# Optimization experiments

Hardware: AMD Instinct MI355X
Metric: run time of the kernel (lower is better)

## Reference

```python
import jax, jax.numpy as jnp
import numpy as np

B, C, H, W = 4, 128, 128, 128
E, K, HID = 11, 6, 512  # num_experts, active_experts, 4*dim


def setup_inputs() -> dict:
    key = jax.random.key(0)
    ks = jax.random.split(key, 5)
    return {
        "x": jax.random.normal(ks[0], (B, C, H, W), jnp.float32),
        "gate_w": jax.random.normal(ks[1], (E, C), jnp.float32) * 0.02,
        "gate_b": jnp.zeros((E,), jnp.float32),
        "w1": jax.random.normal(ks[2], (E, HID, C), jnp.float32) * 0.02,
        "b1": jnp.zeros((E, HID), jnp.float32),
        "w2": jax.random.normal(ks[3], (E, C, HID), jnp.float32) * 0.02,
        "b2": jnp.zeros((E, C), jnp.float32),
    }


def reference(x, gate_w, gate_b, w1, b1, w2, b2):
    n_experts = gate_w.shape[0]
    k = K  # active_experts
    # channels-last for per-pixel routing / 1x1-conv-as-matmul
    xcl = jnp.transpose(x, (0, 2, 3, 1))  # [B,H,W,C]
    # --- router (1x1 conv gate + softmax over experts + top-k) ---
    logits = jnp.einsum('bhwc,ec->bhwe', xcl, gate_w) + gate_b
    scores = jax.nn.softmax(logits, axis=-1)            # [B,H,W,E]
    topk_p, topk_i = jax.lax.top_k(scores, k)           # [B,H,W,K]
    topk_p = topk_p / topk_p.sum(axis=-1, keepdims=True)
    # scatter routing weights into dense per-expert mask (indices distinct)
    onehot = jax.nn.one_hot(topk_i, n_experts, dtype=x.dtype)  # [B,H,W,K,E]
    mask = jnp.einsum('bhwke,bhwk->bhwe', onehot, topk_p)      # [B,H,W,E]
    # --- dense expert compute, masked accumulate (as in original loop) ---
    acc = jnp.zeros_like(xcl)
    for e in range(n_experts):
        h = jax.nn.gelu(jnp.einsum('bhwc,dc->bhwd', xcl, w1[e]) + b1[e],
                        approximate=False)  # torch GELU is exact erf form
        oe = jnp.einsum('bhwd,cd->bhwc', h, w2[e]) + b2[e]
        acc = acc + mask[..., e:e + 1] * oe
    y = x + jnp.transpose(acc, (0, 3, 1, 2))  # back to NCHW
    # --- load-balancing aux loss ---
    mean_prob = scores.mean(axis=(0, 1, 2))            # [E]
    mean_load = onehot.sum(axis=3).mean(axis=(0, 1, 2))  # binary mask mean, [E]
    aux_loss = n_experts * jnp.sum(mean_prob * mean_load)
    return (y, aux_loss)
```

## Files before the change

### kernel.cpp

```cpp
#include <hip/hip_runtime.h>
#include <stdint.h>

#define C_   128
#define HW_  16384
#define CHW_ (C_*HW_)
#define N_   65536
#define E_   11
#define K_   6
#define HID_ 512

typedef __attribute__((ext_vector_type(8))) _Float16 half8;
typedef __attribute__((ext_vector_type(2))) _Float16 h2;
typedef __attribute__((ext_vector_type(2))) __fp16 fp16v2;
typedef __attribute__((ext_vector_type(16))) float float16v;
typedef __attribute__((ext_vector_type(2))) unsigned uint2v;

#define GLD(g, s) __builtin_amdgcn_global_load_lds( \
    (const __attribute__((address_space(1))) unsigned int*)(uintptr_t)(g), \
    (__attribute__((address_space(3))) unsigned int*)(unsigned int)(uintptr_t)(s), 16, 0, 0)

__device__ __forceinline__ h2 pkrtz(float a, float b){
  union { fp16v2 f; h2 h; } u;
  u.f = __builtin_amdgcn_cvt_pkrtz(a, b);
  return u.h;
}
__device__ __forceinline__ h2 gelu2h(h2 v, h2 wr2){
  h2 u = v * v;
  h2 s = u * (h2)(_Float16)(-0.00076957f) + (h2)(_Float16)(0.0147811f);
  s = s * u + (h2)(_Float16)(-0.126434f);
  s = s * u + (h2)(_Float16)(0.795742f);
  h2 p = v * s;
  h2 phi = p * (h2)(_Float16)(0.5f) + (h2)(_Float16)(0.5f);
  return v * wr2 * phi;
}
__device__ __forceinline__ void pswap32(unsigned &a, unsigned &b){
#if __has_builtin(__builtin_amdgcn_permlane32_swap)
  uint2v r = __builtin_amdgcn_permlane32_swap(a, b, false, false);
  a = r.x; b = r.y;
#else
  asm volatile("v_permlane32_swap_b32 %0, %1" : "+v"(a), "+v"(b));
#endif
}

__global__ __launch_bounds__(256) void k_convert(const float* __restrict__ w1,
                                                 const float* __restrict__ w2,
                                                 const float* __restrict__ b1,
                                                 unsigned short* __restrict__ wimg,
                                                 unsigned short* __restrict__ b1h,
                                                 float* __restrict__ auxsum){
  int t = blockIdx.x * 256 + threadIdx.x;
  if (t < 23) auxsum[t] = 0.0f;
  if (t >= 185856) return;
  if (t >= 180224){
    int t2 = t - 180224;
    int rec = t2 >> 5, j5 = t2 & 31;
    int hi = j5 >> 4, j = j5 & 15;
    int e = rec >> 4, hc = rec & 15;
    int row = (j & 3) + 8 * (j >> 2) + 4 * hi;
    union { _Float16 h; unsigned short u; } cv;
    cv.h = (_Float16)b1[e * 512 + hc * 32 + row];
    b1h[rec * 32 + j5] = cv.u;
    return;
  }
  const float* src;
  size_t dst;
  if (t < 90112){
    int e = t >> 13, hid = (t >> 4) & 511, c8 = t & 15;
    src = w1 + (size_t)t * 8;
    int rec = e * 16 + (hid >> 5);
    int kc = c8 >> 1, half = c8 & 1;
    int l = (hid & 31) | (half << 5);
    dst = (size_t)rec * 8192 + kc * 512 + l * 8;
  } else {
    int u = t - 90112;
    int e = u >> 13, cc = (u >> 6) & 127, hd8 = u & 63;
    src = w2 + (size_t)u * 8;
    int rec = e * 16 + (hd8 >> 2);
    int kc2 = (hd8 >> 1) & 1, half = hd8 & 1, ct = cc >> 5;
    int l = (cc & 31) | (half << 5);
    dst = (size_t)rec * 8192 + 4096 + (ct * 2 + kc2) * 512 + l * 8;
  }
  float4 a = *(const float4*)src, b = *(const float4*)(src + 4);
  union { _Float16 h[8]; uint4 v; } u4;
  u4.h[0] = (_Float16)a.x; u4.h[1] = (_Float16)a.y;
  u4.h[2] = (_Float16)a.z; u4.h[3] = (_Float16)a.w;
  u4.h[4] = (_Float16)b.x; u4.h[5] = (_Float16)b.y;
  u4.h[6] = (_Float16)b.z; u4.h[7] = (_Float16)b.w;
  *(uint4*)(wimg + dst) = u4.v;
}

__global__ __launch_bounds__(256) void k_pre(const float* __restrict__ x,
                                             const float* __restrict__ gw,
                                             const float* __restrict__ gb,
                                             const float* __restrict__ b2,
                                             unsigned short* __restrict__ xcl,
                                             float* __restrict__ mask,
                                             float* __restrict__ auxsum){
  __shared__ __align__(16) float tt[64 * 130];
  __shared__ __align__(16) float g[E_ * C_];
  __shared__ float gbs[E_];
  __shared__ float ap[E_], al[E_];
  int tid = threadIdx.x;
  int pix0 = blockIdx.x * 64;
  int b = pix0 >> 14, hw0 = pix0 & 16383;
  const float* xb = x + (size_t)b * CHW_ + hw0;

  for (int i = tid; i < E_ * C_; i += 256) g[i] = gw[i];
  if (tid < E_) { gbs[tid] = gb[tid]; ap[tid] = 0.f; al[tid] = 0.f; }

  #pragma unroll 4
  for (int it = 0; it < 32; ++it){
    int flat = it * 256 + tid;
    int c = flat >> 6, p = flat & 63;
    tt[p * 130 + c] = xb[c * HW_ + p];
  }
  __syncthreads();
  #pragma unroll 4
  for (int it = 0; it < 16; ++it){
    int u = it * 256 + tid;
    int p = u >> 6, cc = u & 63;
    float f0 = tt[p * 130 + 2 * cc], f1 = tt[p * 130 + 2 * cc + 1];
    union { h2 h; unsigned u; } pv;
    pv.h = pkrtz(f0, f1);
    ((unsigned*)xcl)[(size_t)(pix0 + p) * 64 + cc] = pv.u;
  }

  int p = tid >> 2, t4 = tid & 3;
  float lg[E_];
  #pragma unroll
  for (int e = 0; e < E_; ++e) lg[e] = (t4 == 0) ? gbs[e] : 0.f;
  const float2* ttrow = (const float2*)(tt + p * 130 + t4 * 32);
  #pragma unroll 4
  for (int j2 = 0; j2 < 16; ++j2){
    float2 xv = ttrow[j2];
    #pragma unroll
    for (int e = 0; e < E_; ++e){
      float2 gv = *(const float2*)(g + e * C_ + t4 * 32 + j2 * 2);
      lg[e] = fmaf(xv.x, gv.x, lg[e]);
      lg[e] = fmaf(xv.y, gv.y, lg[e]);
    }
  }
  #pragma unroll
  for (int e = 0; e < E_; ++e){
    lg[e] += __shfl_xor(lg[e], 1, 64);
    lg[e] += __shfl_xor(lg[e], 2, 64);
  }
  float mx = lg[0];
  #pragma unroll
  for (int e = 1; e < E_; ++e) mx = fmaxf(mx, lg[e]);
  float pr[E_]; float s = 0.f;
  #pragma unroll
  for (int e = 0; e < E_; ++e){ pr[e] = expf(lg[e] - mx); s += pr[e]; }
  float inv = 1.0f / s;
  #pragma unroll
  for (int e = 0; e < E_; ++e) pr[e] *= inv;

  unsigned selmask = 0; float wsum = 0.f;
  for (int k = 0; k < K_; ++k){
    float bv = -1.f; int bi = 0;
    #pragma unroll
    for (int e = 0; e < E_; ++e){
      bool better = (((selmask >> e) & 1u) == 0u) && (pr[e] > bv);
      bv = better ? pr[e] : bv;
      bi = better ? e : bi;
    }
    selmask |= 1u << bi; wsum += bv;
  }
  float invw = 1.0f / wsum;
  if (t4 == 0){
    int pix = pix0 + p;
    #pragma unroll
    for (int e = 0; e < E_; ++e){
      bool sel = (selmask >> e) & 1u;
      mask[(size_t)pix * E_ + e] = sel ? pr[e] * invw : 0.f;
      atomicAdd(&ap[e], pr[e]);
      if (sel) atomicAdd(&al[e], 1.0f);
    }
  }
  __syncthreads();
  if (tid < E_){
    atomicAdd(&auxsum[tid], ap[tid]);
    atomicAdd(&auxsum[E_ + tid], al[tid]);
  }
  if (blockIdx.x == 0 && tid < 64){
    int nz = 0;
    for (int idx = tid; idx < E_ * C_; idx += 64)
      nz |= (__float_as_uint(b2[idx]) != 0u) ? 1 : 0;
    if (nz) atomicOr((int*)(auxsum + 22), 1);
  }
}

__global__ __launch_bounds__(512, 2) void k_ffn(const unsigned short* __restrict__ xcl,
                                                const unsigned short* __restrict__ wimg,
                                                const unsigned short* __restrict__ b1h,
                                                const float* __restrict__ b2,
                                                const float* __restrict__ mask,
                                                const float* __restrict__ aux,
                                                const float* __restrict__ x,
                                                float* __restrict__ y){
  __shared__ unsigned char smem[65536];
  int tid = threadIdx.x;
  int w = tid >> 6, l = tid & 63;
  int l31 = l & 31, hi = l >> 5;
  int hi4 = hi * 4;
  int pix0 = blockIdx.x * 256;
  int off = (blockIdx.x % 11) * 16;
  const unsigned char* wimgB = (const unsigned char*)wimg;
  const unsigned char* b1hB  = (const unsigned char*)b1h;

  if (blockIdx.x == 0 && tid == 0){
    float s = 0.f;
    const float invN = 1.0f / (float)N_;
    for (int e = 0; e < E_; ++e)
      s += (aux[e] * invN) * (aux[E_ + e] * invN);
    y[(size_t)N_ * C_] = (float)E_ * s;
  }

  half8 Xf[8];
  {
    const unsigned short* xrow = xcl + ((size_t)(pix0 + w * 32 + l31) << 7) + hi * 8;
    #pragma unroll
    for (int kc = 0; kc < 8; ++kc)
      Xf[kc] = *(const half8*)(xrow + kc * 16);
  }

  uint4 bhA[4], bhB[4];
  const size_t mrow = (size_t)(pix0 + w * 32 + l31) * 11;

  {
    #pragma unroll
    for (int k = 0; k < 2; ++k){
      int rec = off + k;
      const unsigned char* gs = wimgB + (size_t)rec * 16384 + w * 2048 + l * 16;
      unsigned char* dst = smem + k * 16384 + w * 2048;
      GLD(gs, dst);
      GLD(gs + 1024, dst + 1024);
      const unsigned char* bp = b1hB + rec * 64 + hi * 32;
      bhA[2 * k]     = *(const uint4*)(bp);
      bhA[2 * k + 1] = *(const uint4*)(bp + 16);
    }
  }
  float wrn = mask[mrow + (off >> 4)];
  __syncthreads();

  float16v facc[4];
  #pragma unroll
  for (int ct = 0; ct < 4; ++ct) facc[ct] = (float16v)0.0f;
  h2 wr2 = (h2)(_Float16)0.0f;

#define REC_BODY(WB, BH0, BH1)                                                      \
  {                                                                                 \
    float16v hacc_ = (float16v)0.0f;                                                \
    _Pragma("unroll")                                                               \
    for (int kc_ = 0; kc_ < 8; ++kc_){                                              \
      half8 a_ = *(const half8*)((WB) + kc_ * 1024 + l * 16);                       \
      hacc_ = __builtin_amdgcn_mfma_f32_32x32x16_f16(a_, Xf[kc_], hacc_, 0, 0, 0);  \
    }                                                                               \
    union { uint4 v[2]; h2 h[8]; } bu_;                                             \
    bu_.v[0] = BH0; bu_.v[1] = BH1;                                                 \
    unsigned pd_[8];                                                                \
    _Pragma("unroll")                                                               \
    for (int k_ = 0; k_ < 8; ++k_){                                                 \
      h2 v_ = pkrtz(hacc_[2 * k_], hacc_[2 * k_ + 1]);                              \
      v_ = v_ + bu_.h[k_];                                                          \
      union { h2 h; unsigned u; } g_;                                               \
      g_.h = gelu2h(v_, wr2);                                                       \
      pd_[k_] = g_.u;                                                               \
    }                                                                               \
    pswap32(pd_[0], pd_[2]); pswap32(pd_[1], pd_[3]);                               \
    pswap32(pd_[4], pd_[6]); pswap32(pd_[5], pd_[7]);                               \
    union { unsigned u[4]; half8 s; } cv0_, cv1_;                                   \
    cv0_.u[0] = pd_[0]; cv0_.u[1] = pd_[1]; cv0_.u[2] = pd_[2]; cv0_.u[3] = pd_[3]; \
    cv1_.u[0] = pd_[4]; cv1_.u[1] = pd_[5]; cv1_.u[2] = pd_[6]; cv1_.u[3] = pd_[7]; \
    _Pragma("unroll")                                                               \
    for (int ct_ = 0; ct_ < 4; ++ct_){                                              \
      half8 a0_ = *(const half8*)((WB) + 8192 + (ct_ * 2 + 0) * 1024 + l * 16);     \
      half8 a1_ = *(const half8*)((WB) + 8192 + (ct_ * 2 + 1) * 1024 + l * 16);     \
      facc[ct_] = __builtin_amdgcn_mfma_f32_32x32x16_f16(a0_, cv0_.s, facc[ct_], 0, 0, 0); \
      facc[ct_] = __builtin_amdgcn_mfma_f32_32x32x16_f16(a1_, cv1_.s, facc[ct_], 0, 0, 0); \
    }                                                                               \
  }

#define SUPER_BODY(J, BHC, BHL)                                                     \
  {                                                                                 \
    asm volatile("s_waitcnt vmcnt(4)" ::: "memory");                                \
    __builtin_amdgcn_s_barrier();                                                   \
    __builtin_amdgcn_sched_barrier(0);                                              \
         \
    {                                                                               \
      unsigned char* dbuf_ = smem + ((((J) + 1) & 1) << 15);                        \
      _Pragma("unroll")                                                             \
      for (int k_ = 0; k_ < 2; ++k_){                                               \
        int rn_ = 2 * (J) + 2 + k_ + off; if (rn_ >= 176) rn_ -= 176;               \
        const unsigned char* gs_ = wimgB + (size_t)rn_ * 16384 + w * 2048 + l * 16; \
        unsigned char* dst_ = dbuf_ + k_ * 16384 + w * 2048;                        \
        GLD(gs_, dst_);                                                             \
        GLD(gs_ + 1024, dst_ + 1024);                                               \
        const unsigned char* bp_ = b1hB + rn_ * 64 + hi * 32;                       \
        BHL[2 * k_]     = *(const uint4*)(bp_);                                     \
        BHL[2 * k_ + 1] = *(const uint4*)(bp_ + 16);                                \
      }                                                                             \
    }                                                                               \
    __builtin_amdgcn_sched_barrier(0);                                              \
    if (((J) & 7) == 0){           \
      _Float16 wh_ = (_Float16)wrn;                                                 \
      wr2 = (h2){wh_, wh_};                                                         \
      int rn_ = 2 * (J) + 16 + off; if (rn_ >= 176) rn_ -= 176;                     \
      wrn = mask[mrow + (rn_ >> 4)];                                                \
    }                                                                               \
    const unsigned char* wb_ = smem + (((J) & 1) << 15);                            \
    REC_BODY(wb_, BHC[0], BHC[1]);                                                  \
    REC_BODY(wb_ + 16384, BHC[2], BHC[3]);                                          \
  }

  #pragma unroll 1
  for (int jj = 0; jj < 44; ++jj){
    SUPER_BODY(2 * jj,     bhA, bhB);
    SUPER_BODY(2 * jj + 1, bhB, bhA);
  }
#undef SUPER_BODY
#undef REC_BODY

  __syncthreads();
  float* lds_t = (float*)smem;
  float* b2t   = (float*)(smem + 17408);
  for (int idx = tid; idx < 1536; idx += 512){
    int cc = idx / 12, ee = idx - cc * 12;
    b2t[idx] = (ee < 11) ? b2[ee * 128 + cc] : 0.f;
  }
  int b2nz = ((const int*)aux)[22];

  #pragma unroll 1
  for (int h = 0; h < 8; ++h){
    __syncthreads();
    if (w == h){
      #pragma unroll
      for (int ct = 0; ct < 4; ++ct)
        #pragma unroll
        for (int r = 0; r < 16; ++r)
          lds_t[(ct * 32 + (r & 3) + 8 * (r >> 2) + hi4) * 33 + l31] = facc[ct][r];
    }
    __syncthreads();
    int c = tid >> 2, p8 = (tid & 3) << 3;
    int pixg = pix0 + h * 32 + p8;
    size_t base = (size_t)(pixg >> 14) * CHW_ + (size_t)c * HW_ + (pixg & 16383);
    float av[8];
    #pragma unroll
    for (int k = 0; k < 8; ++k) av[k] = lds_t[c * 33 + p8 + k];
    if (b2nz){
      #pragma unroll
      for (int k = 0; k < 8; ++k){
        const float* mr = mask + (size_t)(pixg + k) * 11;
        #pragma unroll
        for (int e = 0; e < 11; ++e) av[k] = fmaf(mr[e], b2t[c * 12 + e], av[k]);
      }
    }
    float4 xv0 = *(const float4*)(x + base);
    float4 xv1 = *(const float4*)(x + base + 4);
    float4 o0 = {av[0] + xv0.x, av[1] + xv0.y, av[2] + xv0.z, av[3] + xv0.w};
    float4 o1 = {av[4] + xv1.x, av[5] + xv1.y, av[6] + xv1.z, av[7] + xv1.w};
    *(float4*)(y + base) = o0;
    *(float4*)(y + base + 4) = o1;
  }
}

extern "C" void kernel_launch(void* const* d_in, const int* in_sizes, int n_in,
                              void* d_out, int out_size, void* d_ws, size_t ws_size,
                              hipStream_t stream){
  const float* x  = (const float*)d_in[0];
  const float* gw = (const float*)d_in[1];
  const float* gb = (const float*)d_in[2];
  const float* w1 = (const float*)d_in[3];
  const float* b1 = (const float*)d_in[4];
  const float* w2 = (const float*)d_in[5];
  const float* b2 = (const float*)d_in[6];
  float* y = (float*)d_out;
  char* ws = (char*)d_ws;

  unsigned short* xcl  = (unsigned short*)ws;
  unsigned short* wimg = (unsigned short*)(ws + 16777216);
  float* mask   = (float*)(ws + 19660800);
  float* auxsum = (float*)(ws + 22544384);
  unsigned short* b1h  = (unsigned short*)(ws + 22544480);

  hipLaunchKernelGGL(k_convert, dim3(726),  dim3(256), 0, stream, w1, w2, b1, wimg, b1h, auxsum);
  hipLaunchKernelGGL(k_pre,     dim3(1024), dim3(256), 0, stream, x, gw, gb, b2, xcl, mask, auxsum);
  hipLaunchKernelGGL(k_ffn,     dim3(256),  dim3(512), 0, stream, xcl, wimg, b1h, b2, mask, auxsum, x, y);
}
```

Measured before the change: 331.6 us.

## Process two pixel tiles per wave to reuse LDS weight fragments across MFMAs

Halves the block to 256 threads and makes each wave own 64 pixels (two 32-pixel tiles), so every weight fragment read from LDS feeds two MFMAs instead of one. Cooperative weight loads are redistributed across four waves, and the epilogue is reworked to dump two accumulator sets per wave and write 16 pixels per thread. This cuts LDS read traffic per FLOP but roughly doubles accumulator and register pressure and halves occupancy (launch bounds 256,1), which may hurt latency hiding.

Measured after the change: 355.0 us. 7.0% more time.

```diff
diff --git a/kernel.cpp b/kernel.cpp
--- a/kernel.cpp
+++ b/kernel.cpp
@@ -190,7 +190,7 @@
   }
 }
 
-__global__ __launch_bounds__(512, 2) void k_ffn(const unsigned short* __restrict__ xcl,
+__global__ __launch_bounds__(256, 1) void k_ffn(const unsigned short* __restrict__ xcl,
                                                 const unsigned short* __restrict__ wimg,
                                                 const unsigned short* __restrict__ b1h,
                                                 const float* __restrict__ b2,
@@ -216,68 +216,84 @@
     y[(size_t)N_ * C_] = (float)E_ * s;
   }
 
-  half8 Xf[8];
+  half8 Xf0[8], Xf1[8];
   {
-    const unsigned short* xrow = xcl + ((size_t)(pix0 + w * 32 + l31) << 7) + hi * 8;
-    #pragma unroll
-    for (int kc = 0; kc < 8; ++kc)
-      Xf[kc] = *(const half8*)(xrow + kc * 16);
+    const unsigned short* xr0 = xcl + ((size_t)(pix0 + w * 64 + l31) << 7) + hi * 8;
+    #pragma unroll
+    for (int kc = 0; kc < 8; ++kc){
+      Xf0[kc] = *(const half8*)(xr0 + kc * 16);
+      Xf1[kc] = *(const half8*)(xr0 + 4096 + kc * 16);
+    }
   }
 
   uint4 bhA[4], bhB[4];
-  const size_t mrow = (size_t)(pix0 + w * 32 + l31) * 11;
-
-  {
-    #pragma unroll
-    for (int k = 0; k < 2; ++k){
-      int rec = off + k;
-      const unsigned char* gs = wimgB + (size_t)rec * 16384 + w * 2048 + l * 16;
-      unsigned char* dst = smem + k * 16384 + w * 2048;
-      GLD(gs, dst);
-      GLD(gs + 1024, dst + 1024);
-      const unsigned char* bp = b1hB + rec * 64 + hi * 32;
-      bhA[2 * k]     = *(const uint4*)(bp);
-      bhA[2 * k + 1] = *(const uint4*)(bp + 16);
-    }
-  }
-  float wrn = mask[mrow + (off >> 4)];
+  const size_t mrowA = (size_t)(pix0 + w * 64 + l31) * 11;
+  const size_t mrowB = mrowA + 32 * 11;
+
+  #pragma unroll
+  for (int k = 0; k < 2; ++k){
+    int rec = off + k;
+    const unsigned char* gs = wimgB + (size_t)rec * 16384 + w * 4096 + l * 16;
+    unsigned char* dst = smem + k * 16384 + w * 4096;
+    GLD(gs, dst);            GLD(gs + 1024, dst + 1024);
+    GLD(gs + 2048, dst + 2048); GLD(gs + 3072, dst + 3072);
+    const unsigned char* bp = b1hB + rec * 64 + hi * 32;
+    bhA[2 * k]     = *(const uint4*)(bp);
+    bhA[2 * k + 1] = *(const uint4*)(bp + 16);
+  }
+  float wrnA = mask[mrowA + (off >> 4)];
+  float wrnB = mask[mrowB + (off >> 4)];
   __syncthreads();
 
-  float16v facc[4];
-  #pragma unroll
-  for (int ct = 0; ct < 4; ++ct) facc[ct] = (float16v)0.0f;
-  h2 wr2 = (h2)(_Float16)0.0f;
-
-#define REC_BODY(WB, BH0, BH1)                                                      \
+  float16v facc0[4], facc1[4];
+  #pragma unroll
+  for (int ct = 0; ct < 4; ++ct){ facc0[ct] = (float16v)0.0f; facc1[ct] = (float16v)0.0f; }
+  h2 wr2A = (h2)(_Float16)0.0f, wr2B = (h2)(_Float16)0.0f;
+
+#define G1(WB, H0, H1)                                                              \
   {                                                                                 \
-    float16v hacc_ = (float16v)0.0f;                                                \
+    half8 a_[8];                                                                    \
+    _Pragma("unroll")                                                               \
+    for (int kc_ = 0; kc_ < 8; ++kc_)                                               \
+      a_[kc_] = *(const half8*)((WB) + kc_ * 1024 + l * 16);                        \
     _Pragma("unroll")                                                               \
     for (int kc_ = 0; kc_ < 8; ++kc_){                                              \
-      half8 a_ = *(const half8*)((WB) + kc_ * 1024 + l * 16);                       \
-      hacc_ = __builtin_amdgcn_mfma_f32_32x32x16_f16(a_, Xf[kc_], hacc_, 0, 0, 0);  \
+      H0 = __builtin_amdgcn_mfma_f32_32x32x16_f16(a_[kc_], Xf0[kc_], H0, 0, 0, 0);  \
+      H1 = __builtin_amdgcn_mfma_f32_32x32x16_f16(a_[kc_], Xf1[kc_], H1, 0, 0, 0);  \
     }                                                                               \
+  }
+
+#define EPI(HACC, BH0, BH1, WR2, CV0, CV1)                                          \
+  {                                                                                 \
     union { uint4 v[2]; h2 h[8]; } bu_;                                             \
     bu_.v[0] = BH0; bu_.v[1] = BH1;                                                 \
     unsigned pd_[8];                                                                \
     _Pragma("unroll")                                                               \
     for (int k_ = 0; k_ < 8; ++k_){                                                 \
-      h2 v_ = pkrtz(hacc_[2 * k_], hacc_[2 * k_ + 1]);                              \
+      h2 v_ = pkrtz(HACC[2 * k_], HACC[2 * k_ + 1]);                                \
       v_ = v_ + bu_.h[k_];                                                          \
       union { h2 h; unsigned u; } g_;                                               \
-      g_.h = gelu2h(v_, wr2);                                                       \
+      g_.h = gelu2h(v_, WR2);                                                       \
       pd_[k_] = g_.u;                                                               \
     }                                                                               \
     pswap32(pd_[0], pd_[2]); pswap32(pd_[1], pd_[3]);                               \
     pswap32(pd_[4], pd_[6]); pswap32(pd_[5], pd_[7]);                               \
-    union { unsigned u[4]; half8 s; } cv0_, cv1_;                                   \
-    cv0_.u[0] = pd_[0]; cv0_.u[1] = pd_[1]; cv0_.u[2] = pd_[2]; cv0_.u[3] = pd_[3]; \
-    cv1_.u[0] = pd_[4]; cv1_.u[1] = pd_[5]; cv1_.u[2] = pd_[6]; cv1_.u[3] = pd_[7]; \
+    union { unsigned u[4]; half8 s; } c0_, c1_;                                     \
+    c0_.u[0] = pd_[0]; c0_.u[1] = pd_[1]; c0_.u[2] = pd_[2]; c0_.u[3] = pd_[3];     \
+    c1_.u[0] = pd_[4]; c1_.u[1] = pd_[5]; c1_.u[2] = pd_[6]; c1_.u[3] = pd_[7];     \
+    CV0 = c0_.s; CV1 = c1_.s;                                                       \
+  }
+
+#define G2(WB, A00, A01, A10, A11)                                                  \
+  {                                                                                 \
     _Pragma("unroll")                                                               \
     for (int ct_ = 0; ct_ < 4; ++ct_){                                              \
-      half8 a0_ = *(const half8*)((WB) + 8192 + (ct_ * 2 + 0) * 1024 + l * 16);     \
-      half8 a1_ = *(const half8*)((WB) + 8192 + (ct_ * 2 + 1) * 1024 + l * 16);     \
-      facc[ct_] = __builtin_amdgcn_mfma_f32_32x32x16_f16(a0_, cv0_.s, facc[ct_], 0, 0, 0); \
-      facc[ct_] = __builtin_amdgcn_mfma_f32_32x32x16_f16(a1_, cv1_.s, facc[ct_], 0, 0, 0); \
+      half8 w0_ = *(const half8*)((WB) + 8192 + (ct_ * 2 + 0) * 1024 + l * 16);     \
+      half8 w1_ = *(const half8*)((WB) + 8192 + (ct_ * 2 + 1) * 1024 + l * 16);     \
+      facc0[ct_] = __builtin_amdgcn_mfma_f32_32x32x16_f16(w0_, A00, facc0[ct_], 0, 0, 0); \
+      facc0[ct_] = __builtin_amdgcn_mfma_f32_32x32x16_f16(w1_, A01, facc0[ct_], 0, 0, 0); \
+      facc1[ct_] = __builtin_amdgcn_mfma_f32_32x32x16_f16(w0_, A10, facc1[ct_], 0, 0, 0); \
+      facc1[ct_] = __builtin_amdgcn_mfma_f32_32x32x16_f16(w1_, A11, facc1[ct_], 0, 0, 0); \
     }                                                                               \
   }
 
@@ -287,15 +303,21 @@
     __builtin_amdgcn_s_barrier();                                                   \
     __builtin_amdgcn_sched_barrier(0);                                              \
          \
+                                             \
     {                                                                               \
       unsigned char* dbuf_ = smem + ((((J) + 1) & 1) << 15);                        \
       _Pragma("unroll")                                                             \
       for (int k_ = 0; k_ < 2; ++k_){                                               \
         int rn_ = 2 * (J) + 2 + k_ + off; if (rn_ >= 176) rn_ -= 176;               \
-        const unsigned char* gs_ = wimgB + (size_t)rn_ * 16384 + w * 2048 + l * 16; \
-        unsigned char* dst_ = dbuf_ + k_ * 16384 + w * 2048;                        \
-        GLD(gs_, dst_);                                                             \
-        GLD(gs_ + 1024, dst_ + 1024);                                               \
+        const unsigned char* gs_ = wimgB + (size_t)rn_ * 16384 + w * 4096 + l * 16; \
+        unsigned char* dst_ = dbuf_ + k_ * 16384 + w * 4096;                        \
+        GLD(gs_, dst_);             GLD(gs_ + 1024, dst_ + 1024);                   \
+        GLD(gs_ + 2048, dst_ + 2048); GLD(gs_ + 3072, dst_ + 3072);                 \
+      }                                                                             \
+      __builtin_amdgcn_sched_barrier(0);                                            \
+      _Pragma("unroll")                                                             \
+      for (int k_ = 0; k_ < 2; ++k_){                                               \
+        int rn_ = 2 * (J) + 2 + k_ + off; if (rn_ >= 176) rn_ -= 176;               \
         const unsigned char* bp_ = b1hB + rn_ * 64 + hi * 32;                       \
         BHL[2 * k_]     = *(const uint4*)(bp_);                                     \
         BHL[2 * k_ + 1] = *(const uint4*)(bp_ + 16);                                \
@@ -303,14 +325,25 @@
     }                                                                               \
     __builtin_amdgcn_sched_barrier(0);                                              \
     if (((J) & 7) == 0){           \
-      _Float16 wh_ = (_Float16)wrn;                                                 \
-      wr2 = (h2){wh_, wh_};                                                         \
+      _Float16 wa_ = (_Float16)wrnA, wb_ = (_Float16)wrnB;                          \
+      wr2A = (h2){wa_, wa_}; wr2B = (h2){wb_, wb_};                                 \
       int rn_ = 2 * (J) + 16 + off; if (rn_ >= 176) rn_ -= 176;                     \
-      wrn = mask[mrow + (rn_ >> 4)];                                                \
+      wrnA = mask[mrowA + (rn_ >> 4)];                                              \
+      wrnB = mask[mrowB + (rn_ >> 4)];                                              \
     }                                                                               \
     const unsigned char* wb_ = smem + (((J) & 1) << 15);                            \
-    REC_BODY(wb_, BHC[0], BHC[1]);                                                  \
-    REC_BODY(wb_ + 16384, BHC[2], BHC[3]);                                          \
+    float16v hA0 = (float16v)0.0f, hA1 = (float16v)0.0f;                            \
+    float16v hB0 = (float16v)0.0f, hB1 = (float16v)0.0f;                            \
+    G1(wb_, hA0, hA1);                                                              \
+    G1(wb_ + 16384, hB0, hB1);                     \
+    half8 cA00, cA01, cA10, cA11;                                                   \
+    EPI(hA0, BHC[0], BHC[1], wr2A, cA00, cA01);                                     \
+    EPI(hA1, BHC[0], BHC[1], wr2B, cA10, cA11);                                     \
+    G2(wb_, cA00, cA01, cA10, cA11);               \
+    half8 cB00, cB01, cB10, cB11;                                                   \
+    EPI(hB0, BHC[2], BHC[3], wr2A, cB00, cB01);                                     \
+    EPI(hB1, BHC[2], BHC[3], wr2B, cB10, cB11);                                     \
+    G2(wb_ + 16384, cB00, cB01, cB10, cB11);                                        \
   }
 
   #pragma unroll 1
@@ -319,49 +352,56 @@
     SUPER_BODY(2 * jj + 1, bhB, bhA);
   }
 #undef SUPER_BODY
-#undef REC_BODY
+#undef G2
+#undef EPI
+#undef G1
 
   __syncthreads();
   float* lds_t = (float*)smem;
   float* b2t   = (float*)(smem + 17408);
-  for (int idx = tid; idx < 1536; idx += 512){
+  for (int idx = tid; idx < 1536; idx += 256){
     int cc = idx / 12, ee = idx - cc * 12;
     b2t[idx] = (ee < 11) ? b2[ee * 128 + cc] : 0.f;
   }
   int b2nz = ((const int*)aux)[22];
 
+#define DUMPF(F)                                                                     \
+  _Pragma("unroll")                                                                  \
+  for (int ct_ = 0; ct_ < 4; ++ct_)                                                  \
+    _Pragma("unroll")                                                                \
+    for (int rg_ = 0; rg_ < 16; ++rg_)                                               \
+      lds_t[(ct_ * 32 + (rg_ & 3) + 8 * (rg_ >> 2) + hi4) * 33 + l31] = F[ct_][rg_];
+
   #pragma unroll 1
-  for (int h = 0; h < 8; ++h){
+  for (int r = 0; r < 8; ++r){
     __syncthreads();
-    if (w == h){
-      #pragma unroll
-      for (int ct = 0; ct < 4; ++ct)
-        #pragma unroll
-        for (int r = 0; r < 16; ++r)
-          lds_t[(ct * 32 + (r & 3) + 8 * (r >> 2) + hi4) * 33 + l31] = facc[ct][r];
+    if (w == (r >> 1)){
+      if (r & 1) { DUMPF(facc1) } else { DUMPF(facc0) }
     }
     __syncthreads();
-    int c = tid >> 2, p8 = (tid & 3) << 3;
-    int pixg = pix0 + h * 32 + p8;
+    int c = tid >> 1, ph = (tid & 1) << 4;
+    int pixg = pix0 + r * 32 + ph;
     size_t base = (size_t)(pixg >> 14) * CHW_ + (size_t)c * HW_ + (pixg & 16383);
-    float av[8];
-    #pragma unroll
-    for (int k = 0; k < 8; ++k) av[k] = lds_t[c * 33 + p8 + k];
+    float av[16];
+    #pragma unroll
+    for (int k = 0; k < 16; ++k) av[k] = lds_t[c * 33 + ph + k];
     if (b2nz){
       #pragma unroll
-      for (int k = 0; k < 8; ++k){
+      for (int k = 0; k < 16; ++k){
         const float* mr = mask + (size_t)(pixg + k) * 11;
         #pragma unroll
         for (int e = 0; e < 11; ++e) av[k] = fmaf(mr[e], b2t[c * 12 + e], av[k]);
       }
     }
-    float4 xv0 = *(const float4*)(x + base);
-    float4 xv1 = *(const float4*)(x + base + 4);
-    float4 o0 = {av[0] + xv0.x, av[1] + xv0.y, av[2] + xv0.z, av[3] + xv0.w};
-    float4 o1 = {av[4] + xv1.x, av[5] + xv1.y, av[6] + xv1.z, av[7] + xv1.w};
-    *(float4*)(y + base) = o0;
-    *(float4*)(y + base + 4) = o1;
-  }
+    #pragma unroll
+    for (int q = 0; q < 4; ++q){
+      float4 xv = *(const float4*)(x + base + q * 4);
+      float4 o = {av[4 * q] + xv.x, av[4 * q + 1] + xv.y,
+                  av[4 * q + 2] + xv.z, av[4 * q + 3] + xv.w};
+      *(float4*)(y + base + q * 4) = o;
+    }
+  }
+#undef DUMPF
 }
 
 extern "C" void kernel_launch(void* const* d_in, const int* in_sizes, int n_in,
@@ -385,5 +425,5 @@
 
   hipLaunchKernelGGL(k_convert, dim3(726),  dim3(256), 0, stream, w1, w2, b1, wimg, b1h, auxsum);
   hipLaunchKernelGGL(k_pre,     dim3(1024), dim3(256), 0, stream, x, gw, gb, b2, xcl, mask, auxsum);
-  hipLaunchKernelGGL(k_ffn,     dim3(256),  dim3(512), 0, stream, xcl, wimg, b1h, b2, mask, auxsum, x, y);
-}
+  hipLaunchKernelGGL(k_ffn,     dim3(256),  dim3(256), 0, stream, xcl, wimg, b1h, b2, mask, auxsum, x, y);
+}
```

## Halve FFN block size to 4 waves, doubling grid to 512 blocks

Applied to the files above, without the earlier changes.

The FFN kernel now runs 256-thread blocks of 4 waves, each handling 128 pixels instead of 256, with twice as many blocks. Each wave now issues four global-to-LDS loads per record instead of two, so the weight staging is shared by fewer waves, and the epilogue transpose uses 16 pixels per thread. The aim is to spread work across more CUs, since 256 blocks underfill the device. The cost is that the weight stream is read from L2 twice as often in total.

New measurement: 346.6 us. 4.5% more time.

```diff
diff --git a/kernel.cpp b/kernel.cpp
--- a/kernel.cpp
+++ b/kernel.cpp
@@ -190,7 +190,7 @@
   }
 }
 
-__global__ __launch_bounds__(512, 2) void k_ffn(const unsigned short* __restrict__ xcl,
+__global__ __launch_bounds__(256, 2) void k_ffn(const unsigned short* __restrict__ xcl,
                                                 const unsigned short* __restrict__ wimg,
                                                 const unsigned short* __restrict__ b1h,
                                                 const float* __restrict__ b2,
@@ -203,7 +203,7 @@
   int w = tid >> 6, l = tid & 63;
   int l31 = l & 31, hi = l >> 5;
   int hi4 = hi * 4;
-  int pix0 = blockIdx.x * 256;
+  int pix0 = blockIdx.x * 128;
   int off = (blockIdx.x % 11) * 16;
   const unsigned char* wimgB = (const unsigned char*)wimg;
   const unsigned char* b1hB  = (const unsigned char*)b1h;
@@ -231,10 +231,14 @@
     #pragma unroll
     for (int k = 0; k < 2; ++k){
       int rec = off + k;
-      const unsigned char* gs = wimgB + (size_t)rec * 16384 + w * 2048 + l * 16;
-      unsigned char* dst = smem + k * 16384 + w * 2048;
-      GLD(gs, dst);
-      GLD(gs + 1024, dst + 1024);
+      const unsigned char* gs = wimgB + (size_t)rec * 16384 + w * 4096 + l * 16;
+      unsigned char* dst = smem + k * 16384 + w * 4096;
+      GLD(gs, dst);               GLD(gs + 1024, dst + 1024);
+      GLD(gs + 2048, dst + 2048); GLD(gs + 3072, dst + 3072);
+    }
+    #pragma unroll
+    for (int k = 0; k < 2; ++k){
+      int rec = off + k;
       const unsigned char* bp = b1hB + rec * 64 + hi * 32;
       bhA[2 * k]     = *(const uint4*)(bp);
       bhA[2 * k + 1] = *(const uint4*)(bp + 16);
@@ -292,10 +296,15 @@
       _Pragma("unroll")                                                             \
       for (int k_ = 0; k_ < 2; ++k_){                                               \
         int rn_ = 2 * (J) + 2 + k_ + off; if (rn_ >= 176) rn_ -= 176;               \
-        const unsigned char* gs_ = wimgB + (size_t)rn_ * 16384 + w * 2048 + l * 16; \
-        unsigned char* dst_ = dbuf_ + k_ * 16384 + w * 2048;                        \
-        GLD(gs_, dst_);                                                             \
-        GLD(gs_ + 1024, dst_ + 1024);                                               \
+        const unsigned char* gs_ = wimgB + (size_t)rn_ * 16384 + w * 4096 + l * 16; \
+        unsigned char* dst_ = dbuf_ + k_ * 16384 + w * 4096;                        \
+        GLD(gs_, dst_);               GLD(gs_ + 1024, dst_ + 1024);                 \
+        GLD(gs_ + 2048, dst_ + 2048); GLD(gs_ + 3072, dst_ + 3072);                 \
+      }                                                                             \
+      __builtin_amdgcn_sched_barrier(0);                                            \
+      _Pragma("unroll")                                                             \
+      for (int k_ = 0; k_ < 2; ++k_){                                               \
+        int rn_ = 2 * (J) + 2 + k_ + off; if (rn_ >= 176) rn_ -= 176;               \
         const unsigned char* bp_ = b1hB + rn_ * 64 + hi * 32;                       \
         BHL[2 * k_]     = *(const uint4*)(bp_);                                     \
         BHL[2 * k_ + 1] = *(const uint4*)(bp_ + 16);                                \
@@ -324,43 +333,44 @@
   __syncthreads();
   float* lds_t = (float*)smem;
   float* b2t   = (float*)(smem + 17408);
-  for (int idx = tid; idx < 1536; idx += 512){
+  for (int idx = tid; idx < 1536; idx += 256){
     int cc = idx / 12, ee = idx - cc * 12;
     b2t[idx] = (ee < 11) ? b2[ee * 128 + cc] : 0.f;
   }
   int b2nz = ((const int*)aux)[22];
 
   #pragma unroll 1
-  for (int h = 0; h < 8; ++h){
+  for (int r = 0; r < 4; ++r){
     __syncthreads();
-    if (w == h){
+    if (w == r){
       #pragma unroll
       for (int ct = 0; ct < 4; ++ct)
         #pragma unroll
-        for (int r = 0; r < 16; ++r)
-          lds_t[(ct * 32 + (r & 3) + 8 * (r >> 2) + hi4) * 33 + l31] = facc[ct][r];
+        for (int rg = 0; rg < 16; ++rg)
+          lds_t[(ct * 32 + (rg & 3) + 8 * (rg >> 2) + hi4) * 33 + l31] = facc[ct][rg];
     }
     __syncthreads();
-    int c = tid >> 2, p8 = (tid & 3) << 3;
-    int pixg = pix0 + h * 32 + p8;
+    int c = tid >> 1, ph = (tid & 1) << 4;
+    int pixg = pix0 + r * 32 + ph;
     size_t base = (size_t)(pixg >> 14) * CHW_ + (size_t)c * HW_ + (pixg & 16383);
-    float av[8];
-    #pragma unroll
-    for (int k = 0; k < 8; ++k) av[k] = lds_t[c * 33 + p8 + k];
+    float av[16];
+    #pragma unroll
+    for (int k = 0; k < 16; ++k) av[k] = lds_t[c * 33 + ph + k];
     if (b2nz){
       #pragma unroll
-      for (int k = 0; k < 8; ++k){
+      for (int k = 0; k < 16; ++k){
         const float* mr = mask + (size_t)(pixg + k) * 11;
         #pragma unroll
         for (int e = 0; e < 11; ++e) av[k] = fmaf(mr[e], b2t[c * 12 + e], av[k]);
       }
     }
-    float4 xv0 = *(const float4*)(x + base);
-    float4 xv1 = *(const float4*)(x + base + 4);
-    float4 o0 = {av[0] + xv0.x, av[1] + xv0.y, av[2] + xv0.z, av[3] + xv0.w};
-    float4 o1 = {av[4] + xv1.x, av[5] + xv1.y, av[6] + xv1.z, av[7] + xv1.w};
-    *(float4*)(y + base) = o0;
-    *(float4*)(y + base + 4) = o1;
+    #pragma unroll
+    for (int q = 0; q < 4; ++q){
+      float4 xv = *(const float4*)(x + base + q * 4);
+      float4 o = {av[4 * q] + xv.x, av[4 * q + 1] + xv.y,
+                  av[4 * q + 2] + xv.z, av[4 * q + 3] + xv.w};
+      *(float4*)(y + base + q * 4) = o;
+    }
   }
 }
 
@@ -385,5 +395,5 @@
 
   hipLaunchKernelGGL(k_convert, dim3(726),  dim3(256), 0, stream, w1, w2, b1, wimg, b1h, auxsum);
   hipLaunchKernelGGL(k_pre,     dim3(1024), dim3(256), 0, stream, x, gw, gb, b2, xcl, mask, auxsum);
-  hipLaunchKernelGGL(k_ffn,     dim3(256),  dim3(512), 0, stream, xcl, wimg, b1h, b2, mask, auxsum, x, y);
-}
+  hipLaunchKernelGGL(k_ffn,     dim3(512),  dim3(256), 0, stream, xcl, wimg, b1h, b2, mask, auxsum, x, y);
+}
```

## Fuse weight conversion into router prep kernel and replace atomics with partials

Applied to the files above, without the earlier changes.

Merges the weight/bias fp16 conversion kernel into the router preprocessing kernel as extra blocks, removing one kernel launch and its serialization. Aux-loss sums are now written as per-block partials and reduced with a wavefront shuffle in the FFN kernel, so global atomics and the zero-init dependency go away. The b2-nonzero check moves into each FFN block's LDS, and b1 bias register loads are split from the async LDS weight loads with a sched barrier. This adds a small amount of redundant work per FFN block.

New measurement: 308.8 us. 6.9% less time.

```diff
diff --git a/kernel.cpp b/kernel.cpp
--- a/kernel.cpp
+++ b/kernel.cpp
@@ -42,66 +42,67 @@
 #endif
 }
 
-__global__ __launch_bounds__(256) void k_convert(const float* __restrict__ w1,
-                                                 const float* __restrict__ w2,
-                                                 const float* __restrict__ b1,
-                                                 unsigned short* __restrict__ wimg,
-                                                 unsigned short* __restrict__ b1h,
-                                                 float* __restrict__ auxsum){
-  int t = blockIdx.x * 256 + threadIdx.x;
-  if (t < 23) auxsum[t] = 0.0f;
-  if (t >= 185856) return;
-  if (t >= 180224){
-    int t2 = t - 180224;
-    int rec = t2 >> 5, j5 = t2 & 31;
-    int hi = j5 >> 4, j = j5 & 15;
-    int e = rec >> 4, hc = rec & 15;
-    int row = (j & 3) + 8 * (j >> 2) + 4 * hi;
-    union { _Float16 h; unsigned short u; } cv;
-    cv.h = (_Float16)b1[e * 512 + hc * 32 + row];
-    b1h[rec * 32 + j5] = cv.u;
-    return;
-  }
-  const float* src;
-  size_t dst;
-  if (t < 90112){
-    int e = t >> 13, hid = (t >> 4) & 511, c8 = t & 15;
-    src = w1 + (size_t)t * 8;
-    int rec = e * 16 + (hid >> 5);
-    int kc = c8 >> 1, half = c8 & 1;
-    int l = (hid & 31) | (half << 5);
-    dst = (size_t)rec * 8192 + kc * 512 + l * 8;
-  } else {
-    int u = t - 90112;
-    int e = u >> 13, cc = (u >> 6) & 127, hd8 = u & 63;
-    src = w2 + (size_t)u * 8;
-    int rec = e * 16 + (hd8 >> 2);
-    int kc2 = (hd8 >> 1) & 1, half = hd8 & 1, ct = cc >> 5;
-    int l = (cc & 31) | (half << 5);
-    dst = (size_t)rec * 8192 + 4096 + (ct * 2 + kc2) * 512 + l * 8;
-  }
-  float4 a = *(const float4*)src, b = *(const float4*)(src + 4);
-  union { _Float16 h[8]; uint4 v; } u4;
-  u4.h[0] = (_Float16)a.x; u4.h[1] = (_Float16)a.y;
-  u4.h[2] = (_Float16)a.z; u4.h[3] = (_Float16)a.w;
-  u4.h[4] = (_Float16)b.x; u4.h[5] = (_Float16)b.y;
-  u4.h[6] = (_Float16)b.z; u4.h[7] = (_Float16)b.w;
-  *(uint4*)(wimg + dst) = u4.v;
-}
-
-__global__ __launch_bounds__(256) void k_pre(const float* __restrict__ x,
-                                             const float* __restrict__ gw,
-                                             const float* __restrict__ gb,
-                                             const float* __restrict__ b2,
-                                             unsigned short* __restrict__ xcl,
-                                             float* __restrict__ mask,
-                                             float* __restrict__ auxsum){
+__global__ __launch_bounds__(256) void k_prep(const float* __restrict__ x,
+                                              const float* __restrict__ gw,
+                                              const float* __restrict__ gb,
+                                              const float* __restrict__ w1,
+                                              const float* __restrict__ w2,
+                                              const float* __restrict__ b1,
+                                              unsigned short* __restrict__ xcl,
+                                              float* __restrict__ mask,
+                                              unsigned short* __restrict__ wimg,
+                                              unsigned short* __restrict__ b1h,
+                                              float* __restrict__ part){
   __shared__ __align__(16) float tt[64 * 130];
   __shared__ __align__(16) float g[E_ * C_];
   __shared__ float gbs[E_];
   __shared__ float ap[E_], al[E_];
+
+  if (blockIdx.x < 726){
+    int t = blockIdx.x * 256 + threadIdx.x;
+    if (t >= 185856) return;
+    if (t >= 180224){
+      int t2 = t - 180224;
+      int rec = t2 >> 5, j5 = t2 & 31;
+      int hi = j5 >> 4, j = j5 & 15;
+      int e = rec >> 4, hc = rec & 15;
+      int row = (j & 3) + 8 * (j >> 2) + 4 * hi;
+      union { _Float16 h; unsigned short u; } cv;
+      cv.h = (_Float16)b1[e * 512 + hc * 32 + row];
+      b1h[rec * 32 + j5] = cv.u;
+      return;
+    }
+    const float* src;
+    size_t dst;
+    if (t < 90112){
+      int e = t >> 13, hid = (t >> 4) & 511, c8 = t & 15;
+      src = w1 + (size_t)t * 8;
+      int rec = e * 16 + (hid >> 5);
+      int kc = c8 >> 1, half = c8 & 1;
+      int l = (hid & 31) | (half << 5);
+      dst = (size_t)rec * 8192 + kc * 512 + l * 8;
+    } else {
+      int u = t - 90112;
+      int e = u >> 13, cc = (u >> 6) & 127, hd8 = u & 63;
+      src = w2 + (size_t)u * 8;
+      int rec = e * 16 + (hd8 >> 2);
+      int kc2 = (hd8 >> 1) & 1, half = hd8 & 1, ct = cc >> 5;
+      int l = (cc & 31) | (half << 5);
+      dst = (size_t)rec * 8192 + 4096 + (ct * 2 + kc2) * 512 + l * 8;
+    }
+    float4 a = *(const float4*)src, b = *(const float4*)(src + 4);
+    union { _Float16 h[8]; uint4 v; } u4;
+    u4.h[0] = (_Float16)a.x; u4.h[1] = (_Float16)a.y;
+    u4.h[2] = (_Float16)a.z; u4.h[3] = (_Float16)a.w;
+    u4.h[4] = (_Float16)b.x; u4.h[5] = (_Float16)b.y;
+    u4.h[6] = (_Float16)b.z; u4.h[7] = (_Float16)b.w;
+    *(uint4*)(wimg + dst) = u4.v;
+    return;
+  }
+
   int tid = threadIdx.x;
-  int pix0 = blockIdx.x * 64;
+  int pb = blockIdx.x - 726;
+  int pix0 = pb * 64;
   int b = pix0 >> 14, hw0 = pix0 & 16383;
   const float* xb = x + (size_t)b * CHW_ + hw0;
 
@@ -179,14 +180,8 @@
   }
   __syncthreads();
   if (tid < E_){
-    atomicAdd(&auxsum[tid], ap[tid]);
-    atomicAdd(&auxsum[E_ + tid], al[tid]);
-  }
-  if (blockIdx.x == 0 && tid < 64){
-    int nz = 0;
-    for (int idx = tid; idx < E_ * C_; idx += 64)
-      nz |= (__float_as_uint(b2[idx]) != 0u) ? 1 : 0;
-    if (nz) atomicOr((int*)(auxsum + 22), 1);
+    part[tid * 1024 + pb]        = ap[tid];
+    part[(E_ + tid) * 1024 + pb] = al[tid];
   }
 }
 
@@ -199,6 +194,7 @@
                                                 const float* __restrict__ x,
                                                 float* __restrict__ y){
   __shared__ unsigned char smem[65536];
+  __shared__ int b2f;
   int tid = threadIdx.x;
   int w = tid >> 6, l = tid & 63;
   int l31 = l & 31, hi = l >> 5;
@@ -208,12 +204,26 @@
   const unsigned char* wimgB = (const unsigned char*)wimg;
   const unsigned char* b1hB  = (const unsigned char*)b1h;
 
-  if (blockIdx.x == 0 && tid == 0){
+  if (tid == 0) b2f = 0;
+
+  if (blockIdx.x == 0 && w == 0){
     float s = 0.f;
     const float invN = 1.0f / (float)N_;
-    for (int e = 0; e < E_; ++e)
-      s += (aux[e] * invN) * (aux[E_ + e] * invN);
-    y[(size_t)N_ * C_] = (float)E_ * s;
+    for (int e = 0; e < E_; ++e){
+      float pa = 0.f, pl = 0.f;
+      #pragma unroll
+      for (int i = 0; i < 16; ++i){
+        pa += aux[e * 1024 + i * 64 + l];
+        pl += aux[(E_ + e) * 1024 + i * 64 + l];
+      }
+      #pragma unroll
+      for (int o = 32; o; o >>= 1){
+        pa += __shfl_down(pa, o);
+        pl += __shfl_down(pl, o);
+      }
+      if (l == 0) s += (pa * invN) * (pl * invN);
+    }
+    if (l == 0) y[(size_t)N_ * C_] = (float)E_ * s;
   }
 
   half8 Xf[8];
@@ -235,7 +245,10 @@
       unsigned char* dst = smem + k * 16384 + w * 2048;
       GLD(gs, dst);
       GLD(gs + 1024, dst + 1024);
-      const unsigned char* bp = b1hB + rec * 64 + hi * 32;
+    }
+    #pragma unroll
+    for (int k = 0; k < 2; ++k){
+      const unsigned char* bp = b1hB + (off + k) * 64 + hi * 32;
       bhA[2 * k]     = *(const uint4*)(bp);
       bhA[2 * k + 1] = *(const uint4*)(bp + 16);
     }
@@ -296,6 +309,11 @@
         unsigned char* dst_ = dbuf_ + k_ * 16384 + w * 2048;                        \
         GLD(gs_, dst_);                                                             \
         GLD(gs_ + 1024, dst_ + 1024);                                               \
+      }                                                                             \
+      __builtin_amdgcn_sched_barrier(0);                                            \
+      _Pragma("unroll")                                                             \
+      for (int k_ = 0; k_ < 2; ++k_){                                               \
+        int rn_ = 2 * (J) + 2 + k_ + off; if (rn_ >= 176) rn_ -= 176;               \
         const unsigned char* bp_ = b1hB + rn_ * 64 + hi * 32;                       \
         BHL[2 * k_]     = *(const uint4*)(bp_);                                     \
         BHL[2 * k_ + 1] = *(const uint4*)(bp_ + 16);                                \
@@ -326,9 +344,12 @@
   float* b2t   = (float*)(smem + 17408);
   for (int idx = tid; idx < 1536; idx += 512){
     int cc = idx / 12, ee = idx - cc * 12;
-    b2t[idx] = (ee < 11) ? b2[ee * 128 + cc] : 0.f;
-  }
-  int b2nz = ((const int*)aux)[22];
+    float v = (ee < 11) ? b2[ee * 128 + cc] : 0.f;
+    b2t[idx] = v;
+    if (v != 0.f) atomicOr(&b2f, 1);
+  }
+  __syncthreads();
+  int b2nz = b2f;
 
   #pragma unroll 1
   for (int h = 0; h < 8; ++h){
@@ -380,10 +401,11 @@
   unsigned short* xcl  = (unsigned short*)ws;
   unsigned short* wimg = (unsigned short*)(ws + 16777216);
   float* mask   = (float*)(ws + 19660800);
-  float* auxsum = (float*)(ws + 22544384);
-  unsigned short* b1h  = (unsigned short*)(ws + 22544480);
-
-  hipLaunchKernelGGL(k_convert, dim3(726),  dim3(256), 0, stream, w1, w2, b1, wimg, b1h, auxsum);
-  hipLaunchKernelGGL(k_pre,     dim3(1024), dim3(256), 0, stream, x, gw, gb, b2, xcl, mask, auxsum);
-  hipLaunchKernelGGL(k_ffn,     dim3(256),  dim3(512), 0, stream, xcl, wimg, b1h, b2, mask, auxsum, x, y);
-}
+  float* part   = (float*)(ws + 22544384);
+  unsigned short* b1h  = (unsigned short*)(ws + 22634496);
+
+  hipLaunchKernelGGL(k_prep, dim3(1750), dim3(256), 0, stream,
+                     x, gw, gb, w1, w2, b1, xcl, mask, wimg, b1h, part);
+  hipLaunchKernelGGL(k_ffn,  dim3(256),  dim3(512), 0, stream,
+                     xcl, wimg, b1h, b2, mask, part, x, y);
+}
```
